# Kernel tuning notes

Measured on AMD Instinct MI355X. Metric: run time of the kernel, lower is better.

## Reference

```python
import jax, jax.numpy as jnp
import numpy as np

B, F, H, S, K, L, C = 128, 8192, 8192, 4, 32, 3, 100  # batch, encoded feats, hidden, segments, synapses/seg, hidden layers, classes


def setup_inputs() -> dict:
    key = jax.random.key(0)
    k1, k2, k3, k4, k5, k6 = jax.random.split(key, 6)
    # binary encoded input activations (thermometer-coded tabular features)
    x = jax.random.randint(k1, (B, F), 0, 2).astype(jnp.float32)
    # sign weights in {-1,+1} for each synapse of each segment of each neuron
    signs0 = jnp.where(jax.random.bernoulli(k2, 0.5, (S, H, K)), 1.0, -1.0).astype(jnp.float32)
    signsH = jnp.where(jax.random.bernoulli(k3, 0.5, (L - 1, S, H, K)), 1.0, -1.0).astype(jnp.float32)
    # synapse source indices (irregular connectivity)
    idx0 = jax.random.randint(k4, (S, H, K), 0, F, dtype=jnp.int32)
    idxH = jax.random.randint(k5, (L - 1, S, H, K), 0, H, dtype=jnp.int32)
    # per-layer output connection matrices [L, H, C]
    wout = jax.random.normal(k6, (L, H, C), dtype=jnp.float32) * 0.02
    return {"x": x, "signs0": signs0, "signsH": signsH, "wout": wout,
            "idx0": idx0, "idxH": idxH, "threshold": 8}


def _segment_layer(a, idx, signs, threshold):
    # a: [B, P] prev activations; idx/signs: [S, H, K]
    g = a[:, idx]                                  # [B, S, H, K] irregular gather
    z = jnp.einsum('bshk,shk->bsh', g, signs)      # per-segment summed input
    fired = jnp.any(z >= threshold, axis=1)        # OR over segments -> [B, H]
    return fired.astype(a.dtype)


def reference(x, signs0, signsH, wout, idx0, idxH, threshold):
    thr = jnp.float32(threshold)
    a = _segment_layer(x, idx0, signs0, thr)       # hidden layer 0
    acts = [a]
    for l in range(idxH.shape[0]):                 # remaining hidden layers (fixed small L)
        a = _segment_layer(a, idxH[l], signsH[l], thr)
        acts.append(a)
    # sum class votes from every hidden layer's output connection matrix
    out = jnp.einsum('lbh,lhc->bc', jnp.stack(acts, 0), wout)  # [B, C]
    return out
```

## Files before the change

kernel.cpp:

```cpp
#include <hip/hip_runtime.h>
#include <stdint.h>

#define B 128
#define F 8192
#define H 8192
#define S 4
#define K 32
#define L 3
#define C 100

__global__ void pack_x_kernel(const float* __restrict__ x, uint32_t* __restrict__ xP,
                              float* __restrict__ out) {
    const int zi = blockIdx.x * 128 + threadIdx.x;
    if (zi < B * C) out[zi] = 0.0f;

    const int b = threadIdx.x;
    const int wv = threadIdx.x >> 6;
    const int f0 = blockIdx.x * 32;
    const float4* xr = (const float4*)(x + (size_t)b * F + f0);
    for (int j = 0; j < 8; ++j) {
        const float4 v = xr[j];
        const uint64_t m0 = __ballot(v.x > 0.5f);
        const uint64_t m1 = __ballot(v.y > 0.5f);
        const uint64_t m2 = __ballot(v.z > 0.5f);
        const uint64_t m3 = __ballot(v.w > 0.5f);
        if ((threadIdx.x & 63) == 0) {
            const int f = f0 + 4 * j;
            uint32_t* lo = xP + (size_t)(2 * wv) * F;
            uint32_t* hi = xP + (size_t)(2 * wv + 1) * F;
            lo[f + 0] = (uint32_t)m0;  hi[f + 0] = (uint32_t)(m0 >> 32);
            lo[f + 1] = (uint32_t)m1;  hi[f + 1] = (uint32_t)(m1 >> 32);
            lo[f + 2] = (uint32_t)m2;  hi[f + 2] = (uint32_t)(m2 >> 32);
            lo[f + 3] = (uint32_t)m3;  hi[f + 3] = (uint32_t)(m3 >> 32);
        }
    }
}

__device__ __forceinline__ int load_threshold(const int* p) {
    int v = *p;
    if (v >= (1 << 23)) v = (int)__int_as_float(v);
    return v;
}

__global__ void layer_kernel(const uint32_t* __restrict__ prevP,
                             const int* __restrict__ idx,
                             const float* __restrict__ signs,
                             uint32_t* __restrict__ outP,
                             const int* __restrict__ thrp) {
    __shared__ uint32_t tab[H];
    __shared__ uint32_t isg[S][64 * 33];
    __shared__ uint32_t fbuf[256];
    const int tid  = threadIdx.x;
    const int lane = tid & 63;
    const int sw   = tid >> 6;
    const int w    = blockIdx.x & 3;
    const int hg   = blockIdx.x >> 2;
    const int h    = hg * 64 + lane;
    const int thr  = load_threshold(thrp);

    {
        const int4* src = (const int4*)(prevP + (size_t)w * H);
        int4* dst = (int4*)tab;
#pragma unroll
        for (int i = 0; i < 8; ++i)
            dst[i * 256 + tid] = src[i * 256 + tid];
    }
    {
        const int hrow = tid >> 2;
        const int k0   = (tid & 3) * 8;
#pragma unroll
        for (int s = 0; s < S; ++s) {
            const int4*   ib = (const int4*)(idx   + ((size_t)s * H + hg * 64) * K);
            const float4* sb = (const float4*)(signs + ((size_t)s * H + hg * 64) * K);
            const int4   ia = ib[2 * tid],     ic = ib[2 * tid + 1];
            const float4 sa = sb[2 * tid],     sc = sb[2 * tid + 1];
            uint32_t* dst = &isg[s][hrow * 33 + k0];
            dst[0] = (uint32_t)ia.x | ((uint32_t)__float_as_int(sa.x) & 0x80000000u);
            dst[1] = (uint32_t)ia.y | ((uint32_t)__float_as_int(sa.y) & 0x80000000u);
            dst[2] = (uint32_t)ia.z | ((uint32_t)__float_as_int(sa.z) & 0x80000000u);
            dst[3] = (uint32_t)ia.w | ((uint32_t)__float_as_int(sa.w) & 0x80000000u);
            dst[4] = (uint32_t)ic.x | ((uint32_t)__float_as_int(sc.x) & 0x80000000u);
            dst[5] = (uint32_t)ic.y | ((uint32_t)__float_as_int(sc.y) & 0x80000000u);
            dst[6] = (uint32_t)ic.z | ((uint32_t)__float_as_int(sc.z) & 0x80000000u);
            dst[7] = (uint32_t)ic.w | ((uint32_t)__float_as_int(sc.w) & 0x80000000u);
        }
    }
    __syncthreads();

    uint32_t A[6] = {0, 0, 0, 0, 0, 0};
    uint32_t P[6] = {0, 0, 0, 0, 0, 0};
    const uint32_t* row = &isg[sw][lane * 33];
#pragma unroll
    for (int jc = 0; jc < K; jc += 8) {
        uint32_t iv[8];
#pragma unroll
        for (int j = 0; j < 8; ++j) iv[j] = row[jc + j];
        uint32_t a[8];
#pragma unroll
        for (int j = 0; j < 8; ++j) a[j] = tab[iv[j] & 0xFFFF];
#pragma unroll
        for (int j = 0; j < 8; ++j) {
            const uint32_t pm = ~(uint32_t)((int32_t)iv[j] >> 31);
            uint32_t c = a[j];
#pragma unroll
            for (int i = 0; i < 6; ++i) { const uint32_t t = A[i]; A[i] = t ^ c; c = t & c; }
            c = a[j] & pm;
#pragma unroll
            for (int i = 0; i < 6; ++i) { const uint32_t t = P[i]; P[i] = t ^ c; c = t & c; }
        }
    }

    uint32_t Y[7];
    {
        uint32_t c = 0;
#pragma unroll
        for (int i = 0; i < 7; ++i) {
            const uint32_t ai = (i < 6) ? A[i] : 0u;
            const uint32_t bm = ((thr >> i) & 1) ? 0xFFFFFFFFu : 0u;
            const uint32_t t  = ai ^ bm;
            Y[i] = t ^ c;
            c = (ai & bm) | (t & c);
        }
    }
    uint32_t bw = 0;
#pragma unroll
    for (int i = 0; i < 7; ++i) {
        const uint32_t xx = (i >= 1) ? P[i - 1] : 0u;
        const uint32_t d  = xx ^ Y[i];
        bw = ((~xx) & Y[i]) | ((~d) & bw);
    }
    const uint32_t fired = ~bw;

    fbuf[sw * 64 + lane] = fired;
    __syncthreads();
    if (sw == 0) {
        const uint32_t f = fbuf[lane] | fbuf[64 + lane] |
                           fbuf[128 + lane] | fbuf[192 + lane];
        outP[(size_t)w * H + h] = f;
    }
}

#define NHC 16
#define HCH (H / NHC)

__global__ void final_kernel(const uint32_t* __restrict__ actP,
                             const float* __restrict__ wout,
                             float* __restrict__ out) {
    const int lane = threadIdx.x & 63;
    const int wid  = threadIdx.x >> 6;
    const int hc   = blockIdx.x & (NHC - 1);
    const int bg   = blockIdx.x / NHC;
    const int b    = bg * 4 + wid;
    const int w32  = b >> 5;
    const int bit  = b & 31;

    float acc0 = 0.0f, acc1 = 0.0f;
    const int c1 = 64 + lane;
    const bool c1v = (c1 < C);

    for (int l = 0; l < L; ++l) {
        const uint32_t* aT = actP + ((size_t)l * 4 + w32) * H;
        const float* wl = wout + (size_t)l * H * C;
        for (int r = 0; r < HCH / 64; ++r) {
            const int hbase = hc * HCH + r * 64;
            const uint32_t m = aT[hbase + lane];
            uint64_t hm = __ballot((m >> bit) & 1u);
            while (hm) {
                const int slot = __ffsll((unsigned long long)hm) - 1;
                hm &= hm - 1;
                const float* wr = wl + (size_t)(hbase + slot) * C;
                acc0 += wr[lane];
                if (c1v) acc1 += wr[c1];
            }
        }
    }
    atomicAdd(&out[b * C + lane], acc0);
    if (c1v) atomicAdd(&out[b * C + c1], acc1);
}

extern "C" void kernel_launch(void* const* d_in, const int* in_sizes, int n_in,
                              void* d_out, int out_size, void* d_ws, size_t ws_size,
                              hipStream_t stream) {
    const float* x      = (const float*)d_in[0];
    const float* signs0 = (const float*)d_in[1];
    const float* signsH = (const float*)d_in[2];
    const float* wout   = (const float*)d_in[3];
    const int*   idx0   = (const int*)d_in[4];
    const int*   idxH   = (const int*)d_in[5];
    const int*   thr    = (const int*)d_in[6];
    float* out = (float*)d_out;

    uint32_t* xP   = (uint32_t*)d_ws;
    uint32_t* actP = xP + (size_t)4 * F;

    pack_x_kernel<<<F / 32, 128, 0, stream>>>(x, xP, out);

    layer_kernel<<<512, 256, 0, stream>>>(xP, idx0, signs0, actP, thr);
    layer_kernel<<<512, 256, 0, stream>>>(actP, idxH, signsH,
                                          actP + (size_t)4 * H, thr);
    layer_kernel<<<512, 256, 0, stream>>>(actP + (size_t)4 * H,
                                          idxH + (size_t)S * H * K,
                                          signsH + (size_t)S * H * K,
                                          actP + (size_t)8 * H, thr);

    final_kernel<<<32 * NHC, 256, 0, stream>>>(actP, wout, out);
}
```

Measured before the change: 130.7 us.

## Fuse all phases into one persistent kernel with software grid barriers

Replaces the five separate launches (pack, three layers, final) with a single persistent kernel of 256 blocks that steps through each phase and synchronizes with an atomic-counter grid barrier. Each block now handles two batch-word slices per layer, reusing the staged idx/sign shared-memory table across both, and does two work items in the final phase. The aim is to remove launch gaps and the repeated index/sign staging. The cost is spin-barrier overhead and half as many blocks in flight, which lowers parallelism, plus an extra memset to reset the counter.

```diff
diff --git a/kernel.cpp b/kernel.cpp
--- a/kernel.cpp
+++ b/kernel.cpp
@@ -8,63 +8,71 @@
 #define K 32
 #define L 3
 #define C 100
-
-__global__ void pack_x_kernel(const float* __restrict__ x, uint32_t* __restrict__ xP,
-                              float* __restrict__ out) {
-    const int zi = blockIdx.x * 128 + threadIdx.x;
+#define GRID 256
+
+__device__ __forceinline__ int load_threshold(const int* p) {
+    int v = *p;
+    if (v >= (1 << 23)) v = (int)__int_as_float(v);
+    return v;
+}
+
+__device__ __forceinline__ void grid_barrier(uint32_t* bar, int phase) {
+    __threadfence();
+    __syncthreads();
+    if (threadIdx.x == 0) {
+        __hip_atomic_fetch_add(bar, 1u, __ATOMIC_RELEASE, __HIP_MEMORY_SCOPE_AGENT);
+        const uint32_t target = (uint32_t)GRID * (uint32_t)phase;
+        while (__hip_atomic_load(bar, __ATOMIC_ACQUIRE, __HIP_MEMORY_SCOPE_AGENT) < target)
+            __builtin_amdgcn_s_sleep(2);
+    }
+    __syncthreads();
+    __threadfence();
+}
+
+__device__ void pack_phase(const float* __restrict__ x, uint32_t* __restrict__ xP,
+                           float* __restrict__ out) {
+    const int tid = threadIdx.x;
+    const int zi = blockIdx.x * 256 + tid;
     if (zi < B * C) out[zi] = 0.0f;
 
-    const int b = threadIdx.x;
-    const int wv = threadIdx.x >> 6;
-    const int f0 = blockIdx.x * 32;
+    const int b    = tid & 127;
+    const int half = tid >> 7;
+    const int wlo  = ((tid >> 6) & 1) * 2;
+    const int f0   = blockIdx.x * 32 + half * 16;
     const float4* xr = (const float4*)(x + (size_t)b * F + f0);
-    for (int j = 0; j < 8; ++j) {
+#pragma unroll
+    for (int j = 0; j < 4; ++j) {
         const float4 v = xr[j];
         const uint64_t m0 = __ballot(v.x > 0.5f);
         const uint64_t m1 = __ballot(v.y > 0.5f);
         const uint64_t m2 = __ballot(v.z > 0.5f);
         const uint64_t m3 = __ballot(v.w > 0.5f);
-        if ((threadIdx.x & 63) == 0) {
+        if ((tid & 63) == 0) {
             const int f = f0 + 4 * j;
-            uint32_t* lo = xP + (size_t)(2 * wv) * F;
-            uint32_t* hi = xP + (size_t)(2 * wv + 1) * F;
-            lo[f + 0] = (uint32_t)m0;  hi[f + 0] = (uint32_t)(m0 >> 32);
-            lo[f + 1] = (uint32_t)m1;  hi[f + 1] = (uint32_t)(m1 >> 32);
-            lo[f + 2] = (uint32_t)m2;  hi[f + 2] = (uint32_t)(m2 >> 32);
-            lo[f + 3] = (uint32_t)m3;  hi[f + 3] = (uint32_t)(m3 >> 32);
-        }
-    }
-}
-
-__device__ __forceinline__ int load_threshold(const int* p) {
-    int v = *p;
-    if (v >= (1 << 23)) v = (int)__int_as_float(v);
-    return v;
-}
-
-__global__ void layer_kernel(const uint32_t* __restrict__ prevP,
-                             const int* __restrict__ idx,
-                             const float* __restrict__ signs,
-                             uint32_t* __restrict__ outP,
-                             const int* __restrict__ thrp) {
-    __shared__ uint32_t tab[H];
-    __shared__ uint32_t isg[S][64 * 33];
-    __shared__ uint32_t fbuf[256];
+            xP[(size_t)wlo * F + f + 0]       = (uint32_t)m0;
+            xP[(size_t)(wlo + 1) * F + f + 0] = (uint32_t)(m0 >> 32);
+            xP[(size_t)wlo * F + f + 1]       = (uint32_t)m1;
+            xP[(size_t)(wlo + 1) * F + f + 1] = (uint32_t)(m1 >> 32);
+            xP[(size_t)wlo * F + f + 2]       = (uint32_t)m2;
+            xP[(size_t)(wlo + 1) * F + f + 2] = (uint32_t)(m2 >> 32);
+            xP[(size_t)wlo * F + f + 3]       = (uint32_t)m3;
+            xP[(size_t)(wlo + 1) * F + f + 3] = (uint32_t)(m3 >> 32);
+        }
+    }
+}
+
+__device__ void layer_phase(const uint32_t* __restrict__ prevP,
+                            const int* __restrict__ idx,
+                            const float* __restrict__ signs,
+                            uint32_t* __restrict__ outP, const int thr,
+                            uint32_t* tab, uint32_t* isg, uint32_t* fbuf) {
     const int tid  = threadIdx.x;
     const int lane = tid & 63;
     const int sw   = tid >> 6;
-    const int w    = blockIdx.x & 3;
-    const int hg   = blockIdx.x >> 2;
+    const int hg   = blockIdx.x & 127;
+    const int wb   = blockIdx.x >> 7;
     const int h    = hg * 64 + lane;
-    const int thr  = load_threshold(thrp);
-
-    {
-        const int4* src = (const int4*)(prevP + (size_t)w * H);
-        int4* dst = (int4*)tab;
-#pragma unroll
-        for (int i = 0; i < 8; ++i)
-            dst[i * 256 + tid] = src[i * 256 + tid];
-    }
+
     {
         const int hrow = tid >> 2;
         const int k0   = (tid & 3) * 8;
@@ -72,9 +80,9 @@
         for (int s = 0; s < S; ++s) {
             const int4*   ib = (const int4*)(idx   + ((size_t)s * H + hg * 64) * K);
             const float4* sb = (const float4*)(signs + ((size_t)s * H + hg * 64) * K);
-            const int4   ia = ib[2 * tid],     ic = ib[2 * tid + 1];
-            const float4 sa = sb[2 * tid],     sc = sb[2 * tid + 1];
-            uint32_t* dst = &isg[s][hrow * 33 + k0];
+            const int4   ia = ib[2 * tid],  ic = ib[2 * tid + 1];
+            const float4 sa = sb[2 * tid],  sc = sb[2 * tid + 1];
+            uint32_t* dst = isg + s * (64 * 33) + hrow * 33 + k0;
             dst[0] = (uint32_t)ia.x | ((uint32_t)__float_as_int(sa.x) & 0x80000000u);
             dst[1] = (uint32_t)ia.y | ((uint32_t)__float_as_int(sa.y) & 0x80000000u);
             dst[2] = (uint32_t)ia.z | ((uint32_t)__float_as_int(sa.z) & 0x80000000u);
@@ -85,97 +93,144 @@
             dst[7] = (uint32_t)ic.w | ((uint32_t)__float_as_int(sc.w) & 0x80000000u);
         }
     }
-    __syncthreads();
-
-    uint32_t A[6] = {0, 0, 0, 0, 0, 0};
-    uint32_t P[6] = {0, 0, 0, 0, 0, 0};
-    const uint32_t* row = &isg[sw][lane * 33];
-#pragma unroll
-    for (int jc = 0; jc < K; jc += 8) {
-        uint32_t iv[8];
-#pragma unroll
-        for (int j = 0; j < 8; ++j) iv[j] = row[jc + j];
-        uint32_t a[8];
-#pragma unroll
-        for (int j = 0; j < 8; ++j) a[j] = tab[iv[j] & 0xFFFF];
-#pragma unroll
-        for (int j = 0; j < 8; ++j) {
-            const uint32_t pm = ~(uint32_t)((int32_t)iv[j] >> 31);
-            uint32_t c = a[j];
-#pragma unroll
-            for (int i = 0; i < 6; ++i) { const uint32_t t = A[i]; A[i] = t ^ c; c = t & c; }
-            c = a[j] & pm;
-#pragma unroll
-            for (int i = 0; i < 6; ++i) { const uint32_t t = P[i]; P[i] = t ^ c; c = t & c; }
-        }
-    }
-
-    uint32_t Y[7];
-    {
-        uint32_t c = 0;
+
+#pragma unroll
+    for (int it = 0; it < 2; ++it) {
+        const int w = wb + 2 * it;
+        {
+            const int4* src = (const int4*)(prevP + (size_t)w * H);
+            int4* dst = (int4*)tab;
+#pragma unroll
+            for (int i = 0; i < 8; ++i)
+                dst[i * 256 + tid] = src[i * 256 + tid];
+        }
+        __syncthreads();
+
+        uint32_t A[6] = {0, 0, 0, 0, 0, 0};
+        uint32_t P[6] = {0, 0, 0, 0, 0, 0};
+        const uint32_t* row = isg + sw * (64 * 33) + lane * 33;
+#pragma unroll
+        for (int jc = 0; jc < K; jc += 8) {
+            uint32_t iv[8];
+#pragma unroll
+            for (int j = 0; j < 8; ++j) iv[j] = row[jc + j];
+            uint32_t a[8];
+#pragma unroll
+            for (int j = 0; j < 8; ++j) a[j] = tab[iv[j] & 0xFFFF];
+#pragma unroll
+            for (int j = 0; j < 8; ++j) {
+                const uint32_t pm = ~(uint32_t)((int32_t)iv[j] >> 31);
+                uint32_t c = a[j];
+#pragma unroll
+                for (int i = 0; i < 6; ++i) { const uint32_t t = A[i]; A[i] = t ^ c; c = t & c; }
+                c = a[j] & pm;
+#pragma unroll
+                for (int i = 0; i < 6; ++i) { const uint32_t t = P[i]; P[i] = t ^ c; c = t & c; }
+            }
+        }
+
+        uint32_t Y[7];
+        {
+            uint32_t c = 0;
+#pragma unroll
+            for (int i = 0; i < 7; ++i) {
+                const uint32_t ai = (i < 6) ? A[i] : 0u;
+                const uint32_t bm = ((thr >> i) & 1) ? 0xFFFFFFFFu : 0u;
+                const uint32_t t  = ai ^ bm;
+                Y[i] = t ^ c;
+                c = (ai & bm) | (t & c);
+            }
+        }
+        uint32_t bw = 0;
 #pragma unroll
         for (int i = 0; i < 7; ++i) {
-            const uint32_t ai = (i < 6) ? A[i] : 0u;
-            const uint32_t bm = ((thr >> i) & 1) ? 0xFFFFFFFFu : 0u;
-            const uint32_t t  = ai ^ bm;
-            Y[i] = t ^ c;
-            c = (ai & bm) | (t & c);
-        }
-    }
-    uint32_t bw = 0;
-#pragma unroll
-    for (int i = 0; i < 7; ++i) {
-        const uint32_t xx = (i >= 1) ? P[i - 1] : 0u;
-        const uint32_t d  = xx ^ Y[i];
-        bw = ((~xx) & Y[i]) | ((~d) & bw);
-    }
-    const uint32_t fired = ~bw;
-
-    fbuf[sw * 64 + lane] = fired;
-    __syncthreads();
-    if (sw == 0) {
-        const uint32_t f = fbuf[lane] | fbuf[64 + lane] |
-                           fbuf[128 + lane] | fbuf[192 + lane];
-        outP[(size_t)w * H + h] = f;
+            const uint32_t xx = (i >= 1) ? P[i - 1] : 0u;
+            const uint32_t d  = xx ^ Y[i];
+            bw = ((~xx) & Y[i]) | ((~d) & bw);
+        }
+        const uint32_t fired = ~bw;
+
+        fbuf[sw * 64 + lane] = fired;
+        __syncthreads();
+        if (sw == 0) {
+            const uint32_t fo = fbuf[lane] | fbuf[64 + lane] |
+                                fbuf[128 + lane] | fbuf[192 + lane];
+            outP[(size_t)w * H + h] = fo;
+        }
+        __syncthreads();
     }
 }
 
 #define NHC 16
 #define HCH (H / NHC)
 
-__global__ void final_kernel(const uint32_t* __restrict__ actP,
-                             const float* __restrict__ wout,
-                             float* __restrict__ out) {
+__device__ void final_phase(const uint32_t* __restrict__ actP,
+                            const float* __restrict__ wout,
+                            float* __restrict__ out) {
     const int lane = threadIdx.x & 63;
     const int wid  = threadIdx.x >> 6;
-    const int hc   = blockIdx.x & (NHC - 1);
-    const int bg   = blockIdx.x / NHC;
-    const int b    = bg * 4 + wid;
-    const int w32  = b >> 5;
-    const int bit  = b & 31;
-
-    float acc0 = 0.0f, acc1 = 0.0f;
     const int c1 = 64 + lane;
     const bool c1v = (c1 < C);
 
-    for (int l = 0; l < L; ++l) {
-        const uint32_t* aT = actP + ((size_t)l * 4 + w32) * H;
-        const float* wl = wout + (size_t)l * H * C;
-        for (int r = 0; r < HCH / 64; ++r) {
-            const int hbase = hc * HCH + r * 64;
-            const uint32_t m = aT[hbase + lane];
-            uint64_t hm = __ballot((m >> bit) & 1u);
-            while (hm) {
-                const int slot = __ffsll((unsigned long long)hm) - 1;
-                hm &= hm - 1;
-                const float* wr = wl + (size_t)(hbase + slot) * C;
-                acc0 += wr[lane];
-                if (c1v) acc1 += wr[c1];
+#pragma unroll
+    for (int it = 0; it < 2; ++it) {
+        const int item = blockIdx.x + GRID * it;
+        const int hc = item & (NHC - 1);
+        const int bg = item / NHC;
+        const int b  = bg * 4 + wid;
+        const int w32 = b >> 5;
+        const int bit = b & 31;
+
+        float acc0 = 0.0f, acc1 = 0.0f;
+        for (int l = 0; l < L; ++l) {
+            const uint32_t* aT = actP + ((size_t)l * 4 + w32) * H;
+            const float* wl = wout + (size_t)l * H * C;
+            for (int r = 0; r < HCH / 64; ++r) {
+                const int hbase = hc * HCH + r * 64;
+                const uint32_t m = aT[hbase + lane];
+                uint64_t hm = __ballot((m >> bit) & 1u);
+                while (hm) {
+                    const int slot = __ffsll((unsigned long long)hm) - 1;
+                    hm &= hm - 1;
+                    const float* wr = wl + (size_t)(hbase + slot) * C;
+                    acc0 += wr[lane];
+                    if (c1v) acc1 += wr[c1];
+                }
             }
         }
-    }
-    atomicAdd(&out[b * C + lane], acc0);
-    if (c1v) atomicAdd(&out[b * C + c1], acc1);
+        atomicAdd(&out[b * C + lane], acc0);
+        if (c1v) atomicAdd(&out[b * C + c1], acc1);
+    }
+}
+
+__global__ __launch_bounds__(256, 1)
+void fused_kernel(const float* __restrict__ x,
+                  const float* __restrict__ signs0,
+                  const float* __restrict__ signsH,
+                  const float* __restrict__ wout,
+                  const int* __restrict__ idx0,
+                  const int* __restrict__ idxH,
+                  const int* __restrict__ thrp,
+                  float* __restrict__ out,
+                  uint32_t* __restrict__ bar,
+                  uint32_t* __restrict__ xP,
+                  uint32_t* __restrict__ actP) {
+    __shared__ uint32_t tab[H];
+    __shared__ uint32_t isg[S * 64 * 33];
+    __shared__ uint32_t fbuf[256];
+    const int thr = load_threshold(thrp);
+
+    pack_phase(x, xP, out);
+    grid_barrier(bar, 1);
+    layer_phase(xP, idx0, signs0, actP, thr, tab, isg, fbuf);
+    grid_barrier(bar, 2);
+    layer_phase(actP, idxH, signsH, actP + (size_t)4 * H, thr, tab, isg, fbuf);
+    grid_barrier(bar, 3);
+    layer_phase(actP + (size_t)4 * H,
+                idxH + (size_t)S * H * K, signsH + (size_t)S * H * K,
+                actP + (size_t)8 * H, thr, tab, isg, fbuf);
+    grid_barrier(bar, 4);
+    final_phase(actP, wout, out);
 }
 
 extern "C" void kernel_launch(void* const* d_in, const int* in_sizes, int n_in,
@@ -190,18 +245,11 @@
     const int*   thr    = (const int*)d_in[6];
     float* out = (float*)d_out;
 
-    uint32_t* xP   = (uint32_t*)d_ws;
+    uint32_t* bar  = (uint32_t*)d_ws;
+    uint32_t* xP   = (uint32_t*)((char*)d_ws + 1024);
     uint32_t* actP = xP + (size_t)4 * F;
 
-    pack_x_kernel<<<F / 32, 128, 0, stream>>>(x, xP, out);
-
-    layer_kernel<<<512, 256, 0, stream>>>(xP, idx0, signs0, actP, thr);
-    layer_kernel<<<512, 256, 0, stream>>>(actP, idxH, signsH,
-                                          actP + (size_t)4 * H, thr);
-    layer_kernel<<<512, 256, 0, stream>>>(actP + (size_t)4 * H,
-                                          idxH + (size_t)S * H * K,
-                                          signsH + (size_t)S * H * K,
-                                          actP + (size_t)8 * H, thr);
-
-    final_kernel<<<32 * NHC, 256, 0, stream>>>(actP, wout, out);
-}
+    hipMemsetAsync(bar, 0, 16, stream);
+    fused_kernel<<<GRID, 256, 0, stream>>>(x, signs0, signsH, wout, idx0, idxH,
+                                           thr, out, bar, xP, actP);
+}
```

After: 295.2 us. +125.8%, slower.
